# Kernel optimization log

Measured on AMD Instinct MI355X. Metric: run time of the kernel, lower is better.

## Reference

```python
import jax, jax.numpy as jnp
import numpy as np

H, D, G = 8, 64, 64  # heads, dim_head, slice_num
DIM, INNER = 256, H * D
B, N = 4, 32768
EPS_SLICE = 1e-5
EPS_NORM = 1e-12


def setup_inputs() -> dict:
    key = jax.random.key(0)
    ks = jax.random.split(key, 16)
    s = 0.02
    x = jax.random.normal(ks[0], (B, N, DIM), jnp.float32)
    Wfx = jax.random.normal(ks[1], (INNER, DIM), jnp.float32) * s
    bfx = jnp.zeros((INNER,), jnp.float32)
    Wx = jax.random.normal(ks[2], (INNER, DIM), jnp.float32) * s
    bx = jnp.zeros((INNER,), jnp.float32)
    # orthogonal init for slice projection (G == D here)
    a = jax.random.normal(ks[3], (G, D), jnp.float32)
    q_, _ = jnp.linalg.qr(a.T)
    Wslice = q_.T.astype(jnp.float32)
    bslice = jnp.zeros((G,), jnp.float32)
    temp = jnp.ones((1, H, 1, 1), jnp.float32) * 0.5
    Wq = jax.random.normal(ks[4], (D, D), jnp.float32) * s
    Wk = jax.random.normal(ks[5], (D, D), jnp.float32) * s
    Wv = jax.random.normal(ks[6], (D, D), jnp.float32) * s
    res_scale = jnp.asarray(0.1, jnp.float32)
    attn_scale = jnp.ones((1, H, 1, 1), jnp.float32) * 10.0
    Wout = jax.random.normal(ks[7], (DIM, INNER), jnp.float32) * s
    bout = jnp.zeros((DIM,), jnp.float32)
    return dict(x=x, Wfx=Wfx, bfx=bfx, Wx=Wx, bx=bx, Wslice=Wslice,
                bslice=bslice, temp=temp, Wq=Wq, Wk=Wk, Wv=Wv,
                res_scale=res_scale, attn_scale=attn_scale, Wout=Wout, bout=bout)


def reference(x, Wfx, bfx, Wx, bx, Wslice, bslice, temp, Wq, Wk, Wv,
              res_scale, attn_scale, Wout, bout):
    b, n, _ = x.shape
    # project to per-head features: [b,h,n,d]
    fx = (x @ Wfx.T + bfx).reshape(b, n, H, D).transpose(0, 2, 1, 3)
    xm = (x @ Wx.T + bx).reshape(b, n, H, D).transpose(0, 2, 1, 3)
    # slice routing logits [b,h,n,g], temperature-scaled softmax over slices
    logits = (jnp.einsum('bhnd,gd->bhng', xm, Wslice) + bslice) / temp
    sw = jax.nn.softmax(logits, axis=-1)
    snorm = sw.sum(axis=2)  # [b,h,g]
    # weighted pool of N points into G slice tokens [b,h,g,d]
    st = jnp.einsum('bhnc,bhng->bhgc', fx, sw) / (snorm + EPS_SLICE)[..., None]
    # cross-attention among slice tokens
    q = st @ Wq.T                      # [b,h,g,d]
    kv = st.mean(axis=1)               # [b,g,d] (mean over heads)
    k = kv @ Wk.T                      # [b,g,d]
    v = kv @ Wv.T                      # [b,g,d]
    qn = q / jnp.maximum(jnp.linalg.norm(q, axis=-1, keepdims=True), EPS_NORM)
    kn = k / jnp.maximum(jnp.linalg.norm(k, axis=-1, keepdims=True), EPS_NORM)
    attn = jax.nn.softmax(jnp.einsum('bhgd,bsd->bhgs', qn, kn) * attn_scale, axis=-1)
    out_st = jnp.einsum('bhgs,bsd->bhgd', attn, v) + res_scale * st
    # scatter slice tokens back to points, merge heads
    out_x = jnp.einsum('bhgc,bhng->bhnc', out_st, sw)
    out_x = out_x.transpose(0, 2, 1, 3).reshape(b, n, INNER)
    return out_x @ Wout.T + bout
```

## Files before the change

kernel.cpp:

```cpp
#include <hip/hip_runtime.h>
#include <stdint.h>

#define K_H    8
#define K_D    64
#define K_G    64
#define K_DIM  256
#define K_INNER 512
#define K_B    4
#define K_N    32768

#define XS          264
#define XLDS_BYTES  (64 * XS * 2)
#define BUFA_STR    72
#define BUFA_BYTES  (64 * BUFA_STR * 2)
#define BUF2_STR    40
#define BUF2_BYTES  (64 * BUF2_STR * 2)
#define P1_WAVE_BYTES (BUFA_BYTES + BUF2_BYTES)
#define P1_LDS      (XLDS_BYTES + 8 * P1_WAVE_BYTES)
#define OX_STR      520
#define OX_BYTES    (64 * OX_STR * 2)
#define P3_LDS      (XLDS_BYTES + 8 * BUF2_BYTES + OX_BYTES)
#define P2_LDS      (5 * 64 * 65 * 4 + 2 * 64 * 4)

#define WFX_OFF   0
#define WX_OFF    (512 * 256 * 2)
#define WOUT_OFF  (WX_OFF + 512 * 256 * 2)
#define WSL_OFF   (WOUT_OFF + 256 * 512 * 2)
#define STN_OFF   (WSL_OFF + 64 * 64 * 2)
#define SNORM_OFF (STN_OFF + 4 * 8 * 64 * 64 * 4)
#define OST_OFF   (SNORM_OFF + 4 * 8 * 64 * 4)

#define PART_ST_FLOATS (256 * 8 * 4096)

typedef __attribute__((ext_vector_type(8))) short short8;
typedef __attribute__((ext_vector_type(4))) float f4;
typedef __attribute__((ext_vector_type(4))) unsigned short us4;

static __device__ __forceinline__ f4 MFMA(short8 a, short8 b, f4 c) {
  return __builtin_amdgcn_mfma_f32_16x16x32_bf16(a, b, c, 0, 0, 0);
}
static __device__ __forceinline__ unsigned short f2bf(float f) {
  union { float f; unsigned u; } v; v.f = f;
  unsigned r = v.u + 0x7FFFu + ((v.u >> 16) & 1u);
  return (unsigned short)(r >> 16);
}
static __device__ __forceinline__ us4 pack4(f4 v) {
  us4 p; p[0] = f2bf(v[0]); p[1] = f2bf(v[1]); p[2] = f2bf(v[2]); p[3] = f2bf(v[3]);
  return p;
}
static __device__ __forceinline__ void stage_x(const float* __restrict__ xp,
                                               unsigned short* xlds, int tid) {
#pragma unroll
  for (int j = 0; j < 8; ++j) {
    int fi = j * 2048 + tid * 4;
    f4 v = __builtin_nontemporal_load((const f4*)(xp + fi));
    int row = fi >> 8, col = fi & 255;
    us4 p; p[0] = f2bf(v[0]); p[1] = f2bf(v[1]); p[2] = f2bf(v[2]); p[3] = f2bf(v[3]);
    *(us4*)(xlds + row * XS + col) = p;
  }
}

__global__ void prep_kernel(const float* __restrict__ Wfx, const float* __restrict__ Wx,
                            const float* __restrict__ Wsl, const float* __restrict__ Wout,
                            char* __restrict__ ws) {
  int idx = blockIdx.x * blockDim.x + threadIdx.x;
  int stride = gridDim.x * blockDim.x;
  unsigned short* wfxb  = (unsigned short*)(ws + WFX_OFF);
  unsigned short* wxb   = (unsigned short*)(ws + WX_OFF);
  unsigned short* woutb = (unsigned short*)(ws + WOUT_OFF);
  unsigned short* wslb  = (unsigned short*)(ws + WSL_OFF);
  for (int i = idx; i < 512 * 256; i += stride) wfxb[i] = f2bf(Wfx[i]);
  for (int i = idx; i < 512 * 256; i += stride) wxb[i]  = f2bf(Wx[i]);
  for (int i = idx; i < 256 * 512; i += stride) woutb[i] = f2bf(Wout[i]);
  for (int i = idx; i < 64 * 64; i += stride)   wslb[i] = f2bf(Wsl[i]);
  float* z = (float*)(ws + STN_OFF);
  for (int i = idx; i < 4 * 8 * 64 * 64 + 4 * 8 * 64; i += stride) z[i] = 0.0f;
}

__launch_bounds__(512, 2)
__global__ void pass1_kernel(const float* __restrict__ x,
                             const unsigned short* __restrict__ wfx,
                             const unsigned short* __restrict__ wx,
                             const unsigned short* __restrict__ wsl,
                             const float* __restrict__ bfx,
                             const float* __restrict__ bx,
                             const float* __restrict__ bsl,
                             const float* __restrict__ temp,
                             float* __restrict__ part_st,
                             float* __restrict__ part_sn) {
  extern __shared__ char lds[];
  const int tid = threadIdx.x;
  const int lane = tid & 63;
  const int h = tid >> 6;
  const int l15 = lane & 15;
  const int q = lane >> 4;
  const int b = blockIdx.x >> 6;
  const int blb = blockIdx.x & 63;

  unsigned short* xlds = (unsigned short*)lds;
  unsigned short* bufA = (unsigned short*)(lds + XLDS_BYTES + h * P1_WAVE_BYTES);
  unsigned short* buf2 = bufA + BUFA_BYTES / 2;

  const float inv_t = 1.0f / temp[h];
  float bfx_v[4];
#pragma unroll
  for (int ci = 0; ci < 4; ++ci) bfx_v[ci] = bfx[h * 64 + 16 * ci + l15];
  f4 bx_v[4];
#pragma unroll
  for (int mi = 0; mi < 4; ++mi)
#pragma unroll
    for (int r = 0; r < 4; ++r) bx_v[mi][r] = bx[h * 64 + 16 * mi + 4 * q + r];
  f4 bot[4];
#pragma unroll
  for (int gi = 0; gi < 4; ++gi)
#pragma unroll
    for (int r = 0; r < 4; ++r) bot[gi][r] = bsl[16 * gi + 4 * q + r] * inv_t;

  const f4 fz = {0.f, 0.f, 0.f, 0.f};
  f4 stacc[4][4];
  f4 snacc[4];
#pragma unroll
  for (int i = 0; i < 4; ++i) {
    snacc[i] = fz;
#pragma unroll
    for (int j = 0; j < 4; ++j) stacc[i][j] = fz;
  }

  for (int t = 0; t < 8; ++t) {
    const int n0 = (blb * 8 + t) * 64;
    const float* xp = x + ((size_t)b * K_N + n0) * K_DIM;
    __syncthreads();
    stage_x(xp, xlds, tid);
    __syncthreads();

    f4 accX[4][4];
#pragma unroll
    for (int i = 0; i < 4; ++i)
#pragma unroll
      for (int j = 0; j < 4; ++j) accX[i][j] = fz;
#pragma unroll
    for (int ks = 0; ks < 8; ++ks) {
      short8 xb[4], wa[4];
#pragma unroll
      for (int ni = 0; ni < 4; ++ni)
        xb[ni] = *(const short8*)(xlds + (16 * ni + l15) * XS + 32 * ks + 8 * q);
#pragma unroll
      for (int mi = 0; mi < 4; ++mi)
        wa[mi] = *(const short8*)(wx + (size_t)(h * 64 + 16 * mi + l15) * K_DIM + 32 * ks + 8 * q);
#pragma unroll
      for (int mi = 0; mi < 4; ++mi)
#pragma unroll
        for (int ni = 0; ni < 4; ++ni)
          accX[mi][ni] = MFMA(wa[mi], xb[ni], accX[mi][ni]);
    }
#pragma unroll
    for (int mi = 0; mi < 4; ++mi)
#pragma unroll
      for (int ni = 0; ni < 4; ++ni) {
        f4 v = accX[mi][ni] + bx_v[mi];
        *(us4*)(bufA + (16 * ni + l15) * BUFA_STR + 16 * mi + 4 * q) = pack4(v);
      }

    f4 accL[4][4];
#pragma unroll
    for (int i = 0; i < 4; ++i)
#pragma unroll
      for (int j = 0; j < 4; ++j) accL[i][j] = fz;
#pragma unroll
    for (int kh = 0; kh < 2; ++kh) {
      short8 wsa[4], xmb[4];
#pragma unroll
      for (int gi = 0; gi < 4; ++gi)
        wsa[gi] = *(const short8*)(wsl + (16 * gi + l15) * 64 + 32 * kh + 8 * q);
#pragma unroll
      for (int ni = 0; ni < 4; ++ni)
        xmb[ni] = *(const short8*)(bufA + (16 * ni + l15) * BUFA_STR + 32 * kh + 8 * q);
#pragma unroll
      for (int gi = 0; gi < 4; ++gi)
#pragma unroll
        for (int ni = 0; ni < 4; ++ni)
          accL[gi][ni] = MFMA(wsa[gi], xmb[ni], accL[gi][ni]);
    }
#pragma unroll
    for (int gi = 0; gi < 4; ++gi)
#pragma unroll
      for (int ni = 0; ni < 4; ++ni)
        accL[gi][ni] = accL[gi][ni] * inv_t + bot[gi];

    unsigned swp[4][4][2];
#pragma unroll
    for (int ni = 0; ni < 4; ++ni) {
      float m = -3.0e38f;
#pragma unroll
      for (int gi = 0; gi < 4; ++gi)
#pragma unroll
        for (int r = 0; r < 4; ++r) m = fmaxf(m, accL[gi][ni][r]);
      m = fmaxf(m, __shfl_xor(m, 16));
      m = fmaxf(m, __shfl_xor(m, 32));
      float s = 0.f;
#pragma unroll
      for (int gi = 0; gi < 4; ++gi) {
        f4 e;
#pragma unroll
        for (int r = 0; r < 4; ++r) e[r] = __expf(accL[gi][ni][r] - m);
        accL[gi][ni] = e;
        s += e[0] + e[1] + e[2] + e[3];
      }
      s += __shfl_xor(s, 16);
      s += __shfl_xor(s, 32);
      const float rinv = 1.0f / s;
#pragma unroll
      for (int gi = 0; gi < 4; ++gi) {
        accL[gi][ni] *= rinv;
        snacc[gi] += accL[gi][ni];
        swp[gi][ni][0] = (unsigned)f2bf(accL[gi][ni][0]) | ((unsigned)f2bf(accL[gi][ni][1]) << 16);
        swp[gi][ni][1] = (unsigned)f2bf(accL[gi][ni][2]) | ((unsigned)f2bf(accL[gi][ni][3]) << 16);
      }
    }

    f4 accF[4][4];
#pragma unroll
    for (int i = 0; i < 4; ++i)
#pragma unroll
      for (int j = 0; j < 4; ++j) accF[i][j] = fz;
#pragma unroll
    for (int ks = 0; ks < 8; ++ks) {
      short8 xa[4], wb[4];
#pragma unroll
      for (int mi = 0; mi < 4; ++mi)
        xa[mi] = *(const short8*)(xlds + (16 * mi + l15) * XS + 32 * ks + 8 * q);
#pragma unroll
      for (int ci = 0; ci < 4; ++ci)
        wb[ci] = *(const short8*)(wfx + (size_t)(h * 64 + 16 * ci + l15) * K_DIM + 32 * ks + 8 * q);
#pragma unroll
      for (int mi = 0; mi < 4; ++mi)
#pragma unroll
        for (int ci = 0; ci < 4; ++ci)
          accF[mi][ci] = MFMA(xa[mi], wb[ci], accF[mi][ci]);
    }
#pragma unroll
    for (int mi = 0; mi < 4; ++mi)
#pragma unroll
      for (int ci = 0; ci < 4; ++ci) {
        f4 v = accF[mi][ci] + bfx_v[ci];
        *(us4*)(bufA + (16 * ci + l15) * BUFA_STR + 16 * mi + 4 * q) = pack4(v);
      }

#pragma unroll
    for (int kh = 0; kh < 2; ++kh) {
#pragma unroll
      for (int gi = 0; gi < 4; ++gi)
#pragma unroll
        for (int nn = 0; nn < 2; ++nn) {
          const int ni = 2 * kh + nn;
#pragma unroll
          for (int r = 0; r < 4; ++r) {
            unsigned wv = swp[gi][ni][r >> 1];
            buf2[(16 * gi + 4 * q + r) * BUF2_STR + 16 * nn + l15] =
                (unsigned short)(wv >> (16 * (r & 1)));
          }
        }
      short8 aw[4], bw[4];
#pragma unroll
      for (int mt = 0; mt < 4; ++mt)
        aw[mt] = *(const short8*)(buf2 + (16 * mt + l15) * BUF2_STR + 8 * q);
#pragma unroll
      for (int ct = 0; ct < 4; ++ct)
        bw[ct] = *(const short8*)(bufA + (16 * ct + l15) * BUFA_STR + 32 * kh + 8 * q);
#pragma unroll
      for (int mt = 0; mt < 4; ++mt)
#pragma unroll
        for (int ct = 0; ct < 4; ++ct)
          stacc[mt][ct] = MFMA(aw[mt], bw[ct], stacc[mt][ct]);
    }
  }

  float* stp = part_st + (((size_t)blockIdx.x * 8 + h) << 12);
#pragma unroll
  for (int gi = 0; gi < 4; ++gi)
#pragma unroll
    for (int ci = 0; ci < 4; ++ci)
#pragma unroll
      for (int r = 0; r < 4; ++r)
        __builtin_nontemporal_store(stacc[gi][ci][r],
                                    stp + (16 * gi + 4 * q + r) * 64 + 16 * ci + l15);
  float* snp = part_sn + (((size_t)blockIdx.x * 8 + h) << 6);
#pragma unroll
  for (int gi = 0; gi < 4; ++gi)
#pragma unroll
    for (int r = 0; r < 4; ++r) {
      float vv = snacc[gi][r];
      vv += __shfl_xor(vv, 1);
      vv += __shfl_xor(vv, 2);
      vv += __shfl_xor(vv, 4);
      vv += __shfl_xor(vv, 8);
      if (l15 == 0) __builtin_nontemporal_store(vv, snp + 16 * gi + 4 * q + r);
    }
}

__global__ void reduce_kernel(const float* __restrict__ part_st,
                              const float* __restrict__ part_sn,
                              float* __restrict__ stnum,
                              float* __restrict__ snorm) {
  const int gid = blockIdx.x * blockDim.x + threadIdx.x;
  const int i = gid & 4095;
  const int h = (gid >> 12) & 7;
  const int b = gid >> 15;
  const float* p = part_st + ((((size_t)b * 64) * 8 + h) << 12) + i;
  float s = 0.f;
#pragma unroll 8
  for (int blb = 0; blb < 64; ++blb)
    s += __builtin_nontemporal_load(p + (size_t)blb * (8 * 4096));
  stnum[(((size_t)b * 8 + h) << 12) + i] = s;
  if (gid < 2048) {
    const int g = gid & 63, h2 = (gid >> 6) & 7, b2 = gid >> 9;
    const float* ps = part_sn + ((((size_t)b2 * 64) * 8 + h2) << 6) + g;
    float s2 = 0.f;
#pragma unroll 8
    for (int blb = 0; blb < 64; ++blb)
      s2 += __builtin_nontemporal_load(ps + (size_t)blb * (8 * 64));
    snorm[(((size_t)b2 * 8 + h2) << 6) + g] = s2;
  }
}

__global__ void pass2_kernel(const float* __restrict__ stnum, const float* __restrict__ snorm,
                             const float* __restrict__ Wq, const float* __restrict__ Wk,
                             const float* __restrict__ Wv, const float* __restrict__ attn_scale,
                             const float* __restrict__ res_scale,
                             unsigned short* __restrict__ ostT) {
  extern __shared__ char lds2[];
  float* st = (float*)lds2;
  float* kv = st + 64 * 65;
  float* kk = kv + 64 * 65;
  float* vv = kk + 64 * 65;
  float* qq = vv + 64 * 65;
  float* nk = qq + 64 * 65;
  float* nq = nk + 64;
  const int b = blockIdx.x >> 3, h = blockIdx.x & 7;
  const int tid = threadIdx.x;

  float kvr[16], str[16];
#pragma unroll
  for (int j = 0; j < 16; ++j) kvr[j] = 0.f;
  for (int h2 = 0; h2 < 8; ++h2) {
    const float* np = stnum + ((size_t)b * 8 + h2) * 4096;
    const float* sp = snorm + ((size_t)b * 8 + h2) * 64;
#pragma unroll
    for (int j = 0; j < 16; ++j) {
      int idx = tid + 256 * j;
      int g = idx >> 6;
      float v = np[idx] / (sp[g] + 1e-5f);
      kvr[j] += v;
      if (h2 == h) str[j] = v;
    }
  }
#pragma unroll
  for (int j = 0; j < 16; ++j) {
    int idx = tid + 256 * j;
    int g = idx >> 6, d = idx & 63;
    st[g * 65 + d] = str[j];
    kv[g * 65 + d] = kvr[j] * 0.125f;
  }
  __syncthreads();
#pragma unroll 2
  for (int j = 0; j < 16; ++j) {
    int idx = tid + 256 * j;
    int g = idx >> 6, dp = idx & 63;
    float a1 = 0, a2 = 0, a3 = 0;
    for (int dd = 0; dd < 64; ++dd) {
      float kvv = kv[g * 65 + dd], stv = st[g * 65 + dd];
      a1 += kvv * Wk[dp * 64 + dd];
      a2 += kvv * Wv[dp * 64 + dd];
      a3 += stv * Wq[dp * 64 + dd];
    }
    kk[g * 65 + dp] = a1;
    vv[g * 65 + dp] = a2;
    qq[g * 65 + dp] = a3;
  }
  __syncthreads();
  if (tid < 128) {
    int g = tid & 63;
    const float* p = (tid >= 64) ? qq : kk;
    float s = 0;
    for (int d = 0; d < 64; ++d) { float v = p[g * 65 + d]; s += v * v; }
    float nrm = fmaxf(sqrtf(s), 1e-12f);
    ((tid >= 64) ? nq : nk)[g] = nrm;
  }
  __syncthreads();
  const float scale = attn_scale[h];
  float* at = kv;
#pragma unroll 2
  for (int j = 0; j < 16; ++j) {
    int idx = tid + 256 * j;
    int g = idx >> 6, s2 = idx & 63;
    float a = 0;
    for (int d = 0; d < 64; ++d) a += qq[g * 65 + d] * kk[s2 * 65 + d];
    at[g * 65 + s2] = a * scale / (nq[g] * nk[s2]);
  }
  __syncthreads();
  if (tid < 64) {
    int g = tid;
    float m = -3.0e38f;
    for (int s2 = 0; s2 < 64; ++s2) m = fmaxf(m, at[g * 65 + s2]);
    float ssum = 0;
    for (int s2 = 0; s2 < 64; ++s2) {
      float e = __expf(at[g * 65 + s2] - m);
      at[g * 65 + s2] = e;
      ssum += e;
    }
    float r = 1.f / ssum;
    for (int s2 = 0; s2 < 64; ++s2) at[g * 65 + s2] *= r;
  }
  __syncthreads();
  const float rs = res_scale[0];
#pragma unroll 2
  for (int j = 0; j < 16; ++j) {
    int idx = tid + 256 * j;
    int g = idx >> 6, d = idx & 63;
    float o = 0;
    for (int s2 = 0; s2 < 64; ++s2) o += at[g * 65 + s2] * vv[s2 * 65 + d];
    o += rs * st[g * 65 + d];
    ostT[(((size_t)b * 8 + h) * 64 + d) * 64 + g] = f2bf(o);
  }
}

__launch_bounds__(512, 2)
__global__ void pass3_kernel(const float* __restrict__ x,
                             const unsigned short* __restrict__ wx,
                             const unsigned short* __restrict__ wsl,
                             const unsigned short* __restrict__ wout,
                             const unsigned short* __restrict__ ostT,
                             const float* __restrict__ bx,
                             const float* __restrict__ bsl,
                             const float* __restrict__ temp,
                             const float* __restrict__ bout,
                             float* __restrict__ out) {
  extern __shared__ char lds[];
  const int tid = threadIdx.x;
  const int lane = tid & 63;
  const int h = tid >> 6;
  const int l15 = lane & 15;
  const int q = lane >> 4;
  const int b = blockIdx.x >> 9;
  const int n0 = (blockIdx.x & 511) * 64;

  unsigned short* xlds = (unsigned short*)lds;
  unsigned short* buf = (unsigned short*)(lds + XLDS_BYTES + h * BUF2_BYTES);
  unsigned short* ox = (unsigned short*)(lds + XLDS_BYTES + 8 * BUF2_BYTES);

  const float inv_t = 1.0f / temp[h];
  f4 bx_v[4], bot[4];
#pragma unroll
  for (int mi = 0; mi < 4; ++mi)
#pragma unroll
    for (int r = 0; r < 4; ++r) bx_v[mi][r] = bx[h * 64 + 16 * mi + 4 * q + r];
#pragma unroll
  for (int gi = 0; gi < 4; ++gi)
#pragma unroll
    for (int r = 0; r < 4; ++r) bot[gi][r] = bsl[16 * gi + 4 * q + r] * inv_t;
  float bout_v[2];
#pragma unroll
  for (int nt = 0; nt < 2; ++nt) bout_v[nt] = bout[32 * h + 16 * nt + l15];

  const float* xp = x + ((size_t)b * K_N + n0) * K_DIM;
  stage_x(xp, xlds, tid);
  __syncthreads();

  const f4 fz = {0.f, 0.f, 0.f, 0.f};
  f4 accX[4][4];
#pragma unroll
  for (int i = 0; i < 4; ++i)
#pragma unroll
    for (int j = 0; j < 4; ++j) accX[i][j] = fz;
#pragma unroll
  for (int ks = 0; ks < 8; ++ks) {
    short8 xb[4], wa[4];
#pragma unroll
    for (int ni = 0; ni < 4; ++ni)
      xb[ni] = *(const short8*)(xlds + (16 * ni + l15) * XS + 32 * ks + 8 * q);
#pragma unroll
    for (int mi = 0; mi < 4; ++mi)
      wa[mi] = *(const short8*)(wx + (size_t)(h * 64 + 16 * mi + l15) * K_DIM + 32 * ks + 8 * q);
#pragma unroll
    for (int mi = 0; mi < 4; ++mi)
#pragma unroll
      for (int ni = 0; ni < 4; ++ni)
        accX[mi][ni] = MFMA(wa[mi], xb[ni], accX[mi][ni]);
  }
  f4 accL[4][4];
#pragma unroll
  for (int i = 0; i < 4; ++i)
#pragma unroll
    for (int j = 0; j < 4; ++j) accL[i][j] = fz;
#pragma unroll
  for (int kh = 0; kh < 2; ++kh) {
#pragma unroll
    for (int mm = 0; mm < 2; ++mm) {
      const int mi = 2 * kh + mm;
#pragma unroll
      for (int ni = 0; ni < 4; ++ni) {
        f4 v = accX[mi][ni] + bx_v[mi];
        *(us4*)(buf + (16 * ni + l15) * BUF2_STR + 16 * mm + 4 * q) = pack4(v);
      }
    }
    short8 wsa[4], xmb[4];
#pragma unroll
    for (int gi = 0; gi < 4; ++gi)
      wsa[gi] = *(const short8*)(wsl + (16 * gi + l15) * 64 + 32 * kh + 8 * q);
#pragma unroll
    for (int ni = 0; ni < 4; ++ni)
      xmb[ni] = *(const short8*)(buf + (16 * ni + l15) * BUF2_STR + 8 * q);
#pragma unroll
    for (int gi = 0; gi < 4; ++gi)
#pragma unroll
      for (int ni = 0; ni < 4; ++ni)
        accL[gi][ni] = MFMA(wsa[gi], xmb[ni], accL[gi][ni]);
  }
#pragma unroll
  for (int gi = 0; gi < 4; ++gi)
#pragma unroll
    for (int ni = 0; ni < 4; ++ni)
      accL[gi][ni] = accL[gi][ni] * inv_t + bot[gi];
#pragma unroll
  for (int ni = 0; ni < 4; ++ni) {
    float m = -3.0e38f;
#pragma unroll
    for (int gi = 0; gi < 4; ++gi)
#pragma unroll
      for (int r = 0; r < 4; ++r) m = fmaxf(m, accL[gi][ni][r]);
    m = fmaxf(m, __shfl_xor(m, 16));
    m = fmaxf(m, __shfl_xor(m, 32));
    float s = 0.f;
#pragma unroll
    for (int gi = 0; gi < 4; ++gi) {
      f4 e;
#pragma unroll
      for (int r = 0; r < 4; ++r) e[r] = __expf(accL[gi][ni][r] - m);
      accL[gi][ni] = e;
      s += e[0] + e[1] + e[2] + e[3];
    }
    s += __shfl_xor(s, 16);
    s += __shfl_xor(s, 32);
    const float rinv = 1.0f / s;
#pragma unroll
    for (int gi = 0; gi < 4; ++gi) accL[gi][ni] *= rinv;
  }
  f4 accO[4][4];
#pragma unroll
  for (int i = 0; i < 4; ++i)
#pragma unroll
    for (int j = 0; j < 4; ++j) accO[i][j] = fz;
  const unsigned short* op = ostT + ((size_t)b * 8 + h) * 4096;
#pragma unroll
  for (int kh = 0; kh < 2; ++kh) {
#pragma unroll
    for (int gg = 0; gg < 2; ++gg) {
      const int gi = 2 * kh + gg;
#pragma unroll
      for (int ni = 0; ni < 4; ++ni)
        *(us4*)(buf + (16 * ni + l15) * BUF2_STR + 16 * gg + 4 * q) = pack4(accL[gi][ni]);
    }
    short8 ao[4], bo[4];
#pragma unroll
    for (int mt = 0; mt < 4; ++mt)
      ao[mt] = *(const short8*)(op + (16 * mt + l15) * 64 + 32 * kh + 8 * q);
#pragma unroll
    for (int ni = 0; ni < 4; ++ni)
      bo[ni] = *(const short8*)(buf + (16 * ni + l15) * BUF2_STR + 8 * q);
#pragma unroll
    for (int mt = 0; mt < 4; ++mt)
#pragma unroll
      for (int ni = 0; ni < 4; ++ni)
        accO[mt][ni] = MFMA(ao[mt], bo[ni], accO[mt][ni]);
  }
#pragma unroll
  for (int mi = 0; mi < 4; ++mi)
#pragma unroll
    for (int ni = 0; ni < 4; ++ni)
      *(us4*)(ox + (16 * ni + l15) * OX_STR + h * 64 + 16 * mi + 4 * q) = pack4(accO[mi][ni]);
  __syncthreads();

  f4 accC[4][2];
#pragma unroll
  for (int i = 0; i < 4; ++i)
#pragma unroll
    for (int j = 0; j < 2; ++j) accC[i][j] = fz;
#pragma unroll
  for (int ks = 0; ks < 16; ++ks) {
    short8 ax[4], bw8[2];
#pragma unroll
    for (int mt = 0; mt < 4; ++mt)
      ax[mt] = *(const short8*)(ox + (16 * mt + l15) * OX_STR + 32 * ks + 8 * q);
#pragma unroll
    for (int nt = 0; nt < 2; ++nt)
      bw8[nt] = *(const short8*)(wout + (size_t)(32 * h + 16 * nt + l15) * 512 + 32 * ks + 8 * q);
#pragma unroll
    for (int mt = 0; mt < 4; ++mt)
#pragma unroll
      for (int nt = 0; nt < 2; ++nt)
        accC[mt][nt] = MFMA(ax[mt], bw8[nt], accC[mt][nt]);
  }
  float* op2 = out + ((size_t)b * K_N + n0) * K_DIM;
#pragma unroll
  for (int mt = 0; mt < 4; ++mt)
#pragma unroll
    for (int nt = 0; nt < 2; ++nt) {
      f4 v = accC[mt][nt] + bout_v[nt];
#pragma unroll
      for (int r = 0; r < 4; ++r)
        __builtin_nontemporal_store(
            v[r], op2 + (size_t)(16 * mt + 4 * q + r) * K_DIM + 32 * h + 16 * nt + l15);
    }
}

extern "C" void kernel_launch(void* const* d_in, const int* in_sizes, int n_in,
                              void* d_out, int out_size, void* d_ws, size_t ws_size,
                              hipStream_t stream) {
  const float* x    = (const float*)d_in[0];
  const float* Wfx  = (const float*)d_in[1];
  const float* bfx  = (const float*)d_in[2];
  const float* Wx   = (const float*)d_in[3];
  const float* bx   = (const float*)d_in[4];
  const float* Wsl  = (const float*)d_in[5];
  const float* bsl  = (const float*)d_in[6];
  const float* temp = (const float*)d_in[7];
  const float* Wq   = (const float*)d_in[8];
  const float* Wk   = (const float*)d_in[9];
  const float* Wv   = (const float*)d_in[10];
  const float* rs   = (const float*)d_in[11];
  const float* asc  = (const float*)d_in[12];
  const float* Wout = (const float*)d_in[13];
  const float* bout = (const float*)d_in[14];
  float* out = (float*)d_out;
  char* ws = (char*)d_ws;

  unsigned short* wfxb  = (unsigned short*)(ws + WFX_OFF);
  unsigned short* wxb   = (unsigned short*)(ws + WX_OFF);
  unsigned short* woutb = (unsigned short*)(ws + WOUT_OFF);
  unsigned short* wslb  = (unsigned short*)(ws + WSL_OFF);
  float* stn = (float*)(ws + STN_OFF);
  float* snr = (float*)(ws + SNORM_OFF);
  unsigned short* ostb = (unsigned short*)(ws + OST_OFF);
  float* pst = out;
  float* psn = out + PART_ST_FLOATS;

  (void)hipFuncSetAttribute((const void*)pass1_kernel,
                            hipFuncAttributeMaxDynamicSharedMemorySize, P1_LDS);
  (void)hipFuncSetAttribute((const void*)pass2_kernel,
                            hipFuncAttributeMaxDynamicSharedMemorySize, P2_LDS);
  (void)hipFuncSetAttribute((const void*)pass3_kernel,
                            hipFuncAttributeMaxDynamicSharedMemorySize, P3_LDS);

  prep_kernel<<<256, 256, 0, stream>>>(Wfx, Wx, Wsl, Wout, ws);
  pass1_kernel<<<256, 512, P1_LDS, stream>>>(x, wfxb, wxb, wslb, bfx, bx, bsl, temp,
                                             pst, psn);
  reduce_kernel<<<512, 256, 0, stream>>>(pst, psn, stn, snr);
  pass2_kernel<<<32, 256, P2_LDS, stream>>>(stn, snr, Wq, Wk, Wv, asc, rs, ostb);
  pass3_kernel<<<2048, 512, P3_LDS, stream>>>(x, wxb, wslb, woutb, ostb, bx, bsl, temp, bout, out);
}
```

Baseline: 868.6 us.

## Fold slice projection into Wx to skip xm GEMM, prefetch x tiles

Precomputes Weff = Wslice·Wx_h and beff = Wslice·bx_h + bslice in the prep kernel. Pass1 and pass3 then compute the slice logits directly from x with one K=256 GEMM, removing the xm GEMM, its bf16 LDS round-trip and the second small GEMM. Pass1 also prefetches the next x tile into registers while computing the current one, to overlap global loads with MFMA work. Rounding Weff to bf16 changes numerics slightly, the extra register buffer adds pressure, and the prep kernel no longer zeroes the stn/snorm workspace.

```diff
diff --git a/kernel.cpp b/kernel.cpp
--- a/kernel.cpp
+++ b/kernel.cpp
@@ -62,29 +62,37 @@
 
 __global__ void prep_kernel(const float* __restrict__ Wfx, const float* __restrict__ Wx,
                             const float* __restrict__ Wsl, const float* __restrict__ Wout,
+                            const float* __restrict__ bx, const float* __restrict__ bsl,
                             char* __restrict__ ws) {
   int idx = blockIdx.x * blockDim.x + threadIdx.x;
   int stride = gridDim.x * blockDim.x;
   unsigned short* wfxb  = (unsigned short*)(ws + WFX_OFF);
-  unsigned short* wxb   = (unsigned short*)(ws + WX_OFF);
+  unsigned short* weffb = (unsigned short*)(ws + WX_OFF);
   unsigned short* woutb = (unsigned short*)(ws + WOUT_OFF);
-  unsigned short* wslb  = (unsigned short*)(ws + WSL_OFF);
+  float* beff = (float*)(ws + WSL_OFF);
   for (int i = idx; i < 512 * 256; i += stride) wfxb[i] = f2bf(Wfx[i]);
-  for (int i = idx; i < 512 * 256; i += stride) wxb[i]  = f2bf(Wx[i]);
   for (int i = idx; i < 256 * 512; i += stride) woutb[i] = f2bf(Wout[i]);
-  for (int i = idx; i < 64 * 64; i += stride)   wslb[i] = f2bf(Wsl[i]);
-  float* z = (float*)(ws + STN_OFF);
-  for (int i = idx; i < 4 * 8 * 64 * 64 + 4 * 8 * 64; i += stride) z[i] = 0.0f;
+  for (int i = idx; i < 8 * 64 * 256; i += stride) {
+    int k = i & 255, g = (i >> 8) & 63, hh = i >> 14;
+    float s = 0.f;
+#pragma unroll 8
+    for (int d = 0; d < 64; ++d) s += Wsl[g * 64 + d] * Wx[(size_t)(hh * 64 + d) * 256 + k];
+    weffb[i] = f2bf(s);
+  }
+  for (int i = idx; i < 8 * 64; i += stride) {
+    int g = i & 63, hh = i >> 6;
+    float s = bsl[g];
+    for (int d = 0; d < 64; ++d) s += Wsl[g * 64 + d] * bx[hh * 64 + d];
+    beff[i] = s;
+  }
 }
 
 __launch_bounds__(512, 2)
 __global__ void pass1_kernel(const float* __restrict__ x,
                              const unsigned short* __restrict__ wfx,
-                             const unsigned short* __restrict__ wx,
-                             const unsigned short* __restrict__ wsl,
+                             const unsigned short* __restrict__ weff,
+                             const float* __restrict__ beff,
                              const float* __restrict__ bfx,
-                             const float* __restrict__ bx,
-                             const float* __restrict__ bsl,
                              const float* __restrict__ temp,
                              float* __restrict__ part_st,
                              float* __restrict__ part_sn) {
@@ -105,16 +113,11 @@
   float bfx_v[4];
 #pragma unroll
   for (int ci = 0; ci < 4; ++ci) bfx_v[ci] = bfx[h * 64 + 16 * ci + l15];
-  f4 bx_v[4];
-#pragma unroll
-  for (int mi = 0; mi < 4; ++mi)
-#pragma unroll
-    for (int r = 0; r < 4; ++r) bx_v[mi][r] = bx[h * 64 + 16 * mi + 4 * q + r];
-  f4 bot[4];
+  f4 botg[4];
 #pragma unroll
   for (int gi = 0; gi < 4; ++gi)
 #pragma unroll
-    for (int r = 0; r < 4; ++r) bot[gi][r] = bsl[16 * gi + 4 * q + r] * inv_t;
+    for (int r = 0; r < 4; ++r) botg[gi][r] = beff[h * 64 + 16 * gi + 4 * q + r] * inv_t;
 
   const f4 fz = {0.f, 0.f, 0.f, 0.f};
   f4 stacc[4][4];
@@ -126,66 +129,55 @@
     for (int j = 0; j < 4; ++j) stacc[i][j] = fz;
   }
 
+  const float* xbase = x + ((size_t)b * K_N + blb * 512) * K_DIM;
+  f4 xreg[8];
+#pragma unroll
+  for (int j = 0; j < 8; ++j)
+    xreg[j] = __builtin_nontemporal_load((const f4*)(xbase + j * 2048 + tid * 4));
+
   for (int t = 0; t < 8; ++t) {
-    const int n0 = (blb * 8 + t) * 64;
-    const float* xp = x + ((size_t)b * K_N + n0) * K_DIM;
     __syncthreads();
-    stage_x(xp, xlds, tid);
+#pragma unroll
+    for (int j = 0; j < 8; ++j) {
+      int fi = j * 2048 + tid * 4;
+      int row = fi >> 8, col = fi & 255;
+      us4 p; p[0] = f2bf(xreg[j][0]); p[1] = f2bf(xreg[j][1]);
+      p[2] = f2bf(xreg[j][2]); p[3] = f2bf(xreg[j][3]);
+      *(us4*)(xlds + row * XS + col) = p;
+    }
     __syncthreads();
-
-    f4 accX[4][4];
+    if (t < 7) {
+      const float* xp2 = xbase + (size_t)(t + 1) * 16384;
+#pragma unroll
+      for (int j = 0; j < 8; ++j)
+        xreg[j] = __builtin_nontemporal_load((const f4*)(xp2 + j * 2048 + tid * 4));
+    }
+
+    f4 accL[4][4];
 #pragma unroll
     for (int i = 0; i < 4; ++i)
 #pragma unroll
-      for (int j = 0; j < 4; ++j) accX[i][j] = fz;
+      for (int j = 0; j < 4; ++j) accL[i][j] = fz;
 #pragma unroll
     for (int ks = 0; ks < 8; ++ks) {
-      short8 xb[4], wa[4];
+      short8 xb[4], wl[4];
 #pragma unroll
       for (int ni = 0; ni < 4; ++ni)
         xb[ni] = *(const short8*)(xlds + (16 * ni + l15) * XS + 32 * ks + 8 * q);
 #pragma unroll
-      for (int mi = 0; mi < 4; ++mi)
-        wa[mi] = *(const short8*)(wx + (size_t)(h * 64 + 16 * mi + l15) * K_DIM + 32 * ks + 8 * q);
-#pragma unroll
-      for (int mi = 0; mi < 4; ++mi)
+      for (int gi = 0; gi < 4; ++gi)
+        wl[gi] = *(const short8*)(weff + (size_t)(h * 64 + 16 * gi + l15) * K_DIM + 32 * ks + 8 * q);
+#pragma unroll
+      for (int gi = 0; gi < 4; ++gi)
 #pragma unroll
         for (int ni = 0; ni < 4; ++ni)
-          accX[mi][ni] = MFMA(wa[mi], xb[ni], accX[mi][ni]);
-    }
-#pragma unroll
-    for (int mi = 0; mi < 4; ++mi)
-#pragma unroll
-      for (int ni = 0; ni < 4; ++ni) {
-        f4 v = accX[mi][ni] + bx_v[mi];
-        *(us4*)(bufA + (16 * ni + l15) * BUFA_STR + 16 * mi + 4 * q) = pack4(v);
-      }
-
-    f4 accL[4][4];
-#pragma unroll
-    for (int i = 0; i < 4; ++i)
-#pragma unroll
-      for (int j = 0; j < 4; ++j) accL[i][j] = fz;
-#pragma unroll
-    for (int kh = 0; kh < 2; ++kh) {
-      short8 wsa[4], xmb[4];
-#pragma unroll
-      for (int gi = 0; gi < 4; ++gi)
-        wsa[gi] = *(const short8*)(wsl + (16 * gi + l15) * 64 + 32 * kh + 8 * q);
+          accL[gi][ni] = MFMA(wl[gi], xb[ni], accL[gi][ni]);
+    }
+#pragma unroll
+    for (int gi = 0; gi < 4; ++gi)
 #pragma unroll
       for (int ni = 0; ni < 4; ++ni)
-        xmb[ni] = *(const short8*)(bufA + (16 * ni + l15) * BUFA_STR + 32 * kh + 8 * q);
-#pragma unroll
-      for (int gi = 0; gi < 4; ++gi)
-#pragma unroll
-        for (int ni = 0; ni < 4; ++ni)
-          accL[gi][ni] = MFMA(wsa[gi], xmb[ni], accL[gi][ni]);
-    }
-#pragma unroll
-    for (int gi = 0; gi < 4; ++gi)
-#pragma unroll
-      for (int ni = 0; ni < 4; ++ni)
-        accL[gi][ni] = accL[gi][ni] * inv_t + bot[gi];
+        accL[gi][ni] = accL[gi][ni] * inv_t + botg[gi];
 
     unsigned swp[4][4][2];
 #pragma unroll
@@ -426,12 +418,10 @@
 
 __launch_bounds__(512, 2)
 __global__ void pass3_kernel(const float* __restrict__ x,
-                             const unsigned short* __restrict__ wx,
-                             const unsigned short* __restrict__ wsl,
+                             const unsigned short* __restrict__ weff,
                              const unsigned short* __restrict__ wout,
                              const unsigned short* __restrict__ ostT,
-                             const float* __restrict__ bx,
-                             const float* __restrict__ bsl,
+                             const float* __restrict__ beff,
                              const float* __restrict__ temp,
                              const float* __restrict__ bout,
                              float* __restrict__ out) {
@@ -449,15 +439,11 @@
   unsigned short* ox = (unsigned short*)(lds + XLDS_BYTES + 8 * BUF2_BYTES);
 
   const float inv_t = 1.0f / temp[h];
-  f4 bx_v[4], bot[4];
-#pragma unroll
-  for (int mi = 0; mi < 4; ++mi)
-#pragma unroll
-    for (int r = 0; r < 4; ++r) bx_v[mi][r] = bx[h * 64 + 16 * mi + 4 * q + r];
+  f4 botg[4];
 #pragma unroll
   for (int gi = 0; gi < 4; ++gi)
 #pragma unroll
-    for (int r = 0; r < 4; ++r) bot[gi][r] = bsl[16 * gi + 4 * q + r] * inv_t;
+    for (int r = 0; r < 4; ++r) botg[gi][r] = beff[h * 64 + 16 * gi + 4 * q + r] * inv_t;
   float bout_v[2];
 #pragma unroll
   for (int nt = 0; nt < 2; ++nt) bout_v[nt] = bout[32 * h + 16 * nt + l15];
@@ -467,60 +453,31 @@
   __syncthreads();
 
   const f4 fz = {0.f, 0.f, 0.f, 0.f};
-  f4 accX[4][4];
+  f4 accL[4][4];
 #pragma unroll
   for (int i = 0; i < 4; ++i)
 #pragma unroll
-    for (int j = 0; j < 4; ++j) accX[i][j] = fz;
+    for (int j = 0; j < 4; ++j) accL[i][j] = fz;
 #pragma unroll
   for (int ks = 0; ks < 8; ++ks) {
-    short8 xb[4], wa[4];
+    short8 xb[4], wl[4];
 #pragma unroll
     for (int ni = 0; ni < 4; ++ni)
       xb[ni] = *(const short8*)(xlds + (16 * ni + l15) * XS + 32 * ks + 8 * q);
 #pragma unroll
-    for (int mi = 0; mi < 4; ++mi)
-      wa[mi] = *(const short8*)(wx + (size_t)(h * 64 + 16 * mi + l15) * K_DIM + 32 * ks + 8 * q);
-#pragma unroll
-    for (int mi = 0; mi < 4; ++mi)
+    for (int gi = 0; gi < 4; ++gi)
+      wl[gi] = *(const short8*)(weff + (size_t)(h * 64 + 16 * gi + l15) * K_DIM + 32 * ks + 8 * q);
+#pragma unroll
+    for (int gi = 0; gi < 4; ++gi)
 #pragma unroll
       for (int ni = 0; ni < 4; ++ni)
-        accX[mi][ni] = MFMA(wa[mi], xb[ni], accX[mi][ni]);
-  }
-  f4 accL[4][4];
-#pragma unroll
-  for (int i = 0; i < 4; ++i)
-#pragma unroll
-    for (int j = 0; j < 4; ++j) accL[i][j] = fz;
-#pragma unroll
-  for (int kh = 0; kh < 2; ++kh) {
-#pragma unroll
-    for (int mm = 0; mm < 2; ++mm) {
-      const int mi = 2 * kh + mm;
-#pragma unroll
-      for (int ni = 0; ni < 4; ++ni) {
-        f4 v = accX[mi][ni] + bx_v[mi];
-        *(us4*)(buf + (16 * ni + l15) * BUF2_STR + 16 * mm + 4 * q) = pack4(v);
-      }
-    }
-    short8 wsa[4], xmb[4];
-#pragma unroll
-    for (int gi = 0; gi < 4; ++gi)
-      wsa[gi] = *(const short8*)(wsl + (16 * gi + l15) * 64 + 32 * kh + 8 * q);
+        accL[gi][ni] = MFMA(wl[gi], xb[ni], accL[gi][ni]);
+  }
+#pragma unroll
+  for (int gi = 0; gi < 4; ++gi)
 #pragma unroll
     for (int ni = 0; ni < 4; ++ni)
-      xmb[ni] = *(const short8*)(buf + (16 * ni + l15) * BUF2_STR + 8 * q);
-#pragma unroll
-    for (int gi = 0; gi < 4; ++gi)
-#pragma unroll
-      for (int ni = 0; ni < 4; ++ni)
-        accL[gi][ni] = MFMA(wsa[gi], xmb[ni], accL[gi][ni]);
-  }
-#pragma unroll
-  for (int gi = 0; gi < 4; ++gi)
-#pragma unroll
-    for (int ni = 0; ni < 4; ++ni)
-      accL[gi][ni] = accL[gi][ni] * inv_t + bot[gi];
+      accL[gi][ni] = accL[gi][ni] * inv_t + botg[gi];
 #pragma unroll
   for (int ni = 0; ni < 4; ++ni) {
     float m = -3.0e38f;
@@ -635,9 +592,9 @@
   char* ws = (char*)d_ws;
 
   unsigned short* wfxb  = (unsigned short*)(ws + WFX_OFF);
-  unsigned short* wxb   = (unsigned short*)(ws + WX_OFF);
+  unsigned short* weffb = (unsigned short*)(ws + WX_OFF);
   unsigned short* woutb = (unsigned short*)(ws + WOUT_OFF);
-  unsigned short* wslb  = (unsigned short*)(ws + WSL_OFF);
+  const float* beffp    = (const float*)(ws + WSL_OFF);
   float* stn = (float*)(ws + STN_OFF);
   float* snr = (float*)(ws + SNORM_OFF);
   unsigned short* ostb = (unsigned short*)(ws + OST_OFF);
@@ -651,10 +608,9 @@
   (void)hipFuncSetAttribute((const void*)pass3_kernel,
                             hipFuncAttributeMaxDynamicSharedMemorySize, P3_LDS);
 
-  prep_kernel<<<256, 256, 0, stream>>>(Wfx, Wx, Wsl, Wout, ws);
-  pass1_kernel<<<256, 512, P1_LDS, stream>>>(x, wfxb, wxb, wslb, bfx, bx, bsl, temp,
-                                             pst, psn);
+  prep_kernel<<<256, 256, 0, stream>>>(Wfx, Wx, Wsl, Wout, bx, bsl, ws);
+  pass1_kernel<<<256, 512, P1_LDS, stream>>>(x, wfxb, weffb, beffp, bfx, temp, pst, psn);
   reduce_kernel<<<512, 256, 0, stream>>>(pst, psn, stn, snr);
   pass2_kernel<<<32, 256, P2_LDS, stream>>>(stn, snr, Wq, Wk, Wv, asc, rs, ostb);
-  pass3_kernel<<<2048, 512, P3_LDS, stream>>>(x, wxb, wslb, woutb, ostb, bx, bsl, temp, bout, out);
-}
+  pass3_kernel<<<2048, 512, P3_LDS, stream>>>(x, weffb, woutb, ostb, beffp, temp, bout, out);
+}
```

After: 1.199 ms. +38.1%, slower.
